# Kernel tuning notes

Measured on AMD Instinct MI355X. Metric: run time of the kernel, lower is better.

Reference implementation:

```python
import jax, jax.numpy as jnp
import numpy as np

EMB = 1024
HID = 1536
NE = 8


def setup_inputs() -> dict:
    key = jax.random.key(0)
    ks = jax.random.split(key, 8)
    B, N, E, H, ne = 4, 2048, EMB, HID, NE
    s = 1.0 / np.sqrt(E)
    sh = 1.0 / np.sqrt(H)
    return {
        "x": jax.random.normal(ks[0], (B, N, E), dtype=jnp.float32),
        "Wr": jax.random.uniform(ks[1], (E, ne), minval=-s, maxval=s, dtype=jnp.float32),
        "br": jax.random.uniform(ks[2], (ne,), minval=-s, maxval=s, dtype=jnp.float32),
        "W1": jax.random.uniform(ks[3], (ne, E, H), minval=-s, maxval=s, dtype=jnp.float32),
        "b1": jax.random.uniform(ks[4], (ne, H), minval=-s, maxval=s, dtype=jnp.float32),
        "W2": jax.random.uniform(ks[5], (ne, H, E), minval=-sh, maxval=sh, dtype=jnp.float32),
        "b2": jax.random.uniform(ks[6], (ne, E), minval=-sh, maxval=sh, dtype=jnp.float32),
        "k": 2,
    }


def reference(x, Wr, br, W1, b1, W2, b2, k):
    B, N, E = x.shape
    T = B * N
    ne = Wr.shape[1]
    flat = x.reshape(T, E)
    logits = flat @ Wr + br                      # [T, ne]
    _, topk_idx = jax.lax.top_k(logits, k)       # [T, k]
    # counts[t, e] = number of top-k slots of token t assigned to expert e
    counts = jax.nn.one_hot(topk_idx, ne, dtype=flat.dtype).sum(axis=1)  # [T, ne]
    out = jnp.zeros_like(flat)
    for e in range(ne):  # small fixed loop over experts (structurally distinct weights)
        h = jax.nn.gelu(flat @ W1[e] + b1[e], approximate=False)  # torch nn.GELU = exact erf
        y = h @ W2[e] + b2[e]
        out = out + counts[:, e:e + 1] * y
    out = out / k
    return out.reshape(B, N, E)
```

## Files before the change

### kernel.cpp

```cpp
#include <hip/hip_runtime.h>
#include <hip/hip_bf16.h>
#include <math.h>

#define T_TOK 8192
#define EMB   1024
#define HID   1536
#define NE    8

typedef float  floatx4 __attribute__((ext_vector_type(4)));
typedef __bf16 bf16x8  __attribute__((ext_vector_type(8)));

#define WS_COUNTS   0
#define WS_OFFSETS  1024
#define WS_TOKMAP   8192
#define WS_TOKLIST  270336
#define WS_YBUF     532480
#define WS_W1T      34086912
#define WS_W2T      59252736
#define WS_H        84418560
#define WS_NEEDED   135143424

__device__ __forceinline__ bool wave_sniff_f32(const void* p, int nelem) {
  const unsigned* w = (const unsigned*)p;
  int nw = nelem >> 1; if (nw > 256) nw = 256;
  const int lane = threadIdx.x & 63;
  int pl = 0, nz = 0;
  for (int i = lane; i < nw; i += 64) {
    unsigned v = w[i];
    if (v) { nz++; unsigned ex = (v >> 23) & 255; if (ex >= 100 && ex <= 150) pl++; }
  }
#pragma unroll
  for (int off = 32; off; off >>= 1) { pl += __shfl_xor(pl, off, 64); nz += __shfl_xor(nz, off, 64); }
  return 2 * pl > nz;
}

__device__ __forceinline__ float eload(const void* p, size_t idx, bool f32) {
  return f32 ? ((const float*)p)[idx] : (float)(((const __bf16*)p)[idx]);
}

__device__ __forceinline__ void glds16(const void* g, void* l) {
  __builtin_amdgcn_global_load_lds(
      (const __attribute__((address_space(1))) unsigned int*)g,
      (__attribute__((address_space(3))) unsigned int*)l, 16, 0, 0);
}

__device__ __forceinline__ void transpose_tile(const void* in, __bf16* out,
                                               int K, int N, bool f32,
                                               int t, int lane) {
  const int ntile = N / 64;
  const int e  = t / 384;
  const int r  = t % 384;
  const int kb = r / ntile;
  const int nb = r % ntile;
  const size_t eoff = (size_t)e * (size_t)K * (size_t)N;
  const int k0 = kb * 64 + (lane >> 3) * 8;
  const int n0 = nb * 64 + (lane & 7) * 8;

  if (f32) {
    floatx4 a0[8], a1[8];
#pragma unroll
    for (int i = 0; i < 8; ++i) {
      const float* g = (const float*)in + eoff + (size_t)(k0 + i) * N + n0;
      a0[i] = *(const floatx4*)g;
      a1[i] = *(const floatx4*)(g + 4);
    }
#pragma unroll
    for (int j = 0; j < 8; ++j) {
      bf16x8 o;
#pragma unroll
      for (int i = 0; i < 8; ++i)
        o[i] = (__bf16)(j < 4 ? a0[i][j] : a1[i][j - 4]);
      *(bf16x8*)(out + eoff + (size_t)(n0 + j) * K + k0) = o;
    }
  } else {
    bf16x8 a[8];
#pragma unroll
    for (int i = 0; i < 8; ++i)
      a[i] = *(const bf16x8*)((const __bf16*)in + eoff + (size_t)(k0 + i) * N + n0);
#pragma unroll
    for (int j = 0; j < 8; ++j) {
      bf16x8 o;
#pragma unroll
      for (int i = 0; i < 8; ++i) o[i] = a[i][j];
      *(bf16x8*)(out + eoff + (size_t)(n0 + j) * K + k0) = o;
    }
  }
}

__global__ __launch_bounds__(256)
void prep_kernel(const void* __restrict__ W1, __bf16* __restrict__ w1t,
                 const void* __restrict__ x, const void* __restrict__ Wr,
                 const void* __restrict__ br, const int* __restrict__ kptr,
                 int* __restrict__ tokmap, __bf16* __restrict__ xbf) {
  const int bid = blockIdx.x;
  const int tid = threadIdx.x;
  const int wave = tid >> 6;
  const int lane = tid & 63;

  if (bid < 768) {
    const bool f32 = wave_sniff_f32(W1, NE * EMB * HID);
    transpose_tile(W1, w1t, EMB, HID, f32, bid * 4 + wave, lane);
    return;
  }

  const bool xf32  = wave_sniff_f32(x, T_TOK * EMB);
  const bool wrf32 = wave_sniff_f32(Wr, EMB * NE);
  const bool brf32 = wave_sniff_f32(br, NE);
  const int t = (bid - 768) * 4 + wave;

  float xv[16];
  {
    size_t base = (size_t)t * EMB + lane * 16;
    if (xf32) {
      const float* g = (const float*)x + base;
#pragma unroll
      for (int c = 0; c < 4; ++c) {
        float4 v = *(const float4*)(g + c * 4);
        xv[c * 4 + 0] = v.x; xv[c * 4 + 1] = v.y; xv[c * 4 + 2] = v.z; xv[c * 4 + 3] = v.w;
      }
    } else {
      bf16x8 u = *(const bf16x8*)((const __bf16*)x + base);
      bf16x8 v = *(const bf16x8*)((const __bf16*)x + base + 8);
#pragma unroll
      for (int j = 0; j < 8; ++j) { xv[j] = (float)u[j]; xv[8 + j] = (float)v[j]; }
    }
  }
  {
    bf16x8 o0, o1;
#pragma unroll
    for (int j = 0; j < 8; ++j) { o0[j] = (__bf16)xv[j]; o1[j] = (__bf16)xv[8 + j]; }
    __bf16* xo = xbf + (size_t)t * EMB + lane * 16;
    *(bf16x8*)xo = o0;
    *(bf16x8*)(xo + 8) = o1;
  }
  float acc[NE];
#pragma unroll
  for (int e = 0; e < NE; ++e) acc[e] = 0.f;
  if (wrf32) {
#pragma unroll
    for (int j = 0; j < 16; ++j) {
      const float* wr = (const float*)Wr + (size_t)(lane * 16 + j) * NE;
#pragma unroll
      for (int e = 0; e < NE; ++e) acc[e] += xv[j] * wr[e];
    }
  } else {
#pragma unroll
    for (int j = 0; j < 16; ++j) {
      bf16x8 wr = *(const bf16x8*)((const __bf16*)Wr + (size_t)(lane * 16 + j) * NE);
#pragma unroll
      for (int e = 0; e < NE; ++e) acc[e] += xv[j] * (float)wr[e];
    }
  }
#pragma unroll
  for (int e = 0; e < NE; ++e) {
#pragma unroll
    for (int off = 32; off > 0; off >>= 1)
      acc[e] += __shfl_xor(acc[e], off, 64);
  }
  if (lane == 0) {
    int k = kptr[0];
    if (k < 1) k = 1; if (k > NE) k = NE;
    float lg[NE];
#pragma unroll
    for (int e = 0; e < NE; ++e) lg[e] = acc[e] + eload(br, e, brf32);
    for (int s = 0; s < k; ++s) {
      int bi = 0; float bv = lg[0];
#pragma unroll
      for (int e = 1; e < NE; ++e) { if (lg[e] > bv) { bv = lg[e]; bi = e; } }
      lg[bi] = -3.0e38f;
      tokmap[t * 8 + s] = bi;
    }
  }
}

__global__ __launch_bounds__(1024)
void bin_kernel(const int* __restrict__ kptr, int* __restrict__ tokmap,
                int* __restrict__ tok_list, int* __restrict__ counts,
                int* __restrict__ offsets) {
  __shared__ int lcnt[NE];
  __shared__ int soff[NE + 1];
  const int tid = threadIdx.x;
  if (tid < NE) lcnt[tid] = 0;
  __syncthreads();
  int k = kptr[0];
  if (k < 1) k = 1; if (k > NE) k = NE;
  for (int t = tid; t < T_TOK; t += 1024) {
    for (int s = 0; s < k; ++s) {
      int e = tokmap[t * 8 + s] & 7;
      int pos = atomicAdd(&lcnt[e], 1);
      tok_list[e * T_TOK + pos] = t;
      tokmap[t * 8 + s] = (e << 16) | pos;
    }
  }
  __syncthreads();
  if (tid == 0) {
    int s = 0;
    for (int e = 0; e < NE; ++e) { soff[e] = s; s += lcnt[e]; }
    soff[NE] = s;
  }
  __syncthreads();
  if (tid < NE) counts[tid] = lcnt[tid];
  if (tid <= NE) offsets[tid] = soff[tid];
  for (int e = 0; e < NE; ++e) {
    const int c = lcnt[e];
    const int end = (c + 127) & ~127;
    for (int i = c + tid; i < end; i += 1024) tok_list[e * T_TOK + i] = 0;
  }
}

__global__ __launch_bounds__(256, 4)
void gemm1_kernel(const __bf16* __restrict__ xbf, const __bf16* __restrict__ w1t,
                  const void* __restrict__ b1, const int* __restrict__ counts,
                  const int* __restrict__ offsets, const int* __restrict__ tok_list,
                  __bf16* __restrict__ hbuf,
                  const void* __restrict__ W2, __bf16* __restrict__ w2t) {
  const int bid = blockIdx.x;
  const int lane = threadIdx.x & 63;

  if (bid < 768) {
    const bool f32 = wave_sniff_f32(W2, NE * EMB * HID);
    transpose_tile(W2, w2t, HID, EMB, f32, bid * 4 + (threadIdx.x >> 6), lane);
    return;
  }

  const int flat = bid - 768;
  const int e   = flat & 7;
  const int idx = flat >> 3;
  const int g   = idx / 12;
  const int nT  = idx % 12;
  const int cnt = counts[e];
  const bool b1f32 = wave_sniff_f32(b1, NE * HID);

  __shared__ __align__(16) __bf16 As[128 * 64];
  __shared__ __align__(16) __bf16 Bs[128 * 64];

  const int wave = threadIdx.x >> 6;
  const int lrow = lane >> 3;
  const int cgs  = (lane & 7) ^ lrow;

  int Rst[4];
#pragma unroll
  for (int q = 0; q < 4; ++q) Rst[q] = (q * 4 + wave) * 8 + lrow;

  const __bf16* pB[4];
#pragma unroll
  for (int q = 0; q < 4; ++q)
    pB[q] = w1t + ((size_t)e * HID + nT * 128 + Rst[q]) * EMB + cgs * 8;

  const int wm = (wave & 1) * 64;
  const int wn = (wave >> 1) * 64;
  const int fr = lane & 15;
  const int fc = lane >> 4;
  int aOff0[4], aOff1[4], bOff0[4], bOff1[4];
#pragma unroll
  for (int i = 0; i < 4; ++i) {
    int R = wm + i * 16 + fr;
    aOff0[i] = R * 128 + (((fc)     ^ (R & 7)) << 4);
    aOff1[i] = R * 128 + (((fc + 4) ^ (R & 7)) << 4);
  }
#pragma unroll
  for (int j = 0; j < 4; ++j) {
    int R = wn + j * 16 + fr;
    bOff0[j] = R * 128 + (((fc)     ^ (R & 7)) << 4);
    bOff1[j] = R * 128 + (((fc + 4) ^ (R & 7)) << 4);
  }

  const int colBase = nT * 128 + wn + fr;
  float bv[4];
#pragma unroll
  for (int j = 0; j < 4; ++j) bv[j] = eload(b1, (size_t)e * HID + colBase + j * 16, b1f32);

  for (int mT = g; mT * 128 < cnt; mT += 16) {
    const __bf16* pA[4];
#pragma unroll
    for (int q = 0; q < 4; ++q) {
      const int tok = tok_list[e * T_TOK + mT * 128 + Rst[q]];
      pA[q] = xbf + (size_t)tok * EMB + cgs * 8;
    }

    floatx4 acc[4][4];
#pragma unroll
    for (int i = 0; i < 4; ++i)
#pragma unroll
      for (int j = 0; j < 4; ++j) acc[i][j] = (floatx4){0.f, 0.f, 0.f, 0.f};

    for (int kb = 0; kb < EMB / 64; ++kb) {
      __syncthreads();
#pragma unroll
      for (int q = 0; q < 4; ++q) glds16(pA[q] + (size_t)kb * 64, As + (q * 4 + wave) * 512);
#pragma unroll
      for (int q = 0; q < 4; ++q) glds16(pB[q] + (size_t)kb * 64, Bs + (q * 4 + wave) * 512);
      __syncthreads();
      bf16x8 af[4], bfr[4];
#pragma unroll
      for (int i = 0; i < 4; ++i) af[i]  = *(const bf16x8*)((const char*)As + aOff0[i]);
#pragma unroll
      for (int j = 0; j < 4; ++j) bfr[j] = *(const bf16x8*)((const char*)Bs + bOff0[j]);
#pragma unroll
      for (int i = 0; i < 4; ++i)
#pragma unroll
        for (int j = 0; j < 4; ++j)
          acc[i][j] = __builtin_amdgcn_mfma_f32_16x16x32_bf16(af[i], bfr[j], acc[i][j], 0, 0, 0);
#pragma unroll
      for (int i = 0; i < 4; ++i) af[i]  = *(const bf16x8*)((const char*)As + aOff1[i]);
#pragma unroll
      for (int j = 0; j < 4; ++j) bfr[j] = *(const bf16x8*)((const char*)Bs + bOff1[j]);
#pragma unroll
      for (int i = 0; i < 4; ++i)
#pragma unroll
        for (int j = 0; j < 4; ++j)
          acc[i][j] = __builtin_amdgcn_mfma_f32_16x16x32_bf16(af[i], bfr[j], acc[i][j], 0, 0, 0);
    }

    const int hBase = offsets[e] + mT * 128;
#pragma unroll
    for (int i = 0; i < 4; ++i) {
      const int rowLoc = wm + i * 16 + fc * 4;
#pragma unroll
      for (int r = 0; r < 4; ++r) {
        const int row = rowLoc + r;
        if (mT * 128 + row < cnt) {
          __bf16* hp = hbuf + (size_t)(hBase + row) * HID + colBase;
#pragma unroll
          for (int j = 0; j < 4; ++j) {
            float v = acc[i][j][r] + bv[j];
            float gl = 0.5f * v * (1.0f + erff(v * 0.70710678118654752f));
            hp[j * 16] = (__bf16)gl;
          }
        }
      }
    }
  }
}

__global__ __launch_bounds__(256, 4)
void gemm2_kernel(const __bf16* __restrict__ hbuf, const __bf16* __restrict__ w2t,
                  const void* __restrict__ b2, const int* __restrict__ counts,
                  const int* __restrict__ offsets, __bf16* __restrict__ ybuf) {
  const int flat = blockIdx.x;
  const int e   = flat & 7;
  const int idx = flat >> 3;
  const int g   = idx >> 3;
  const int nT  = idx & 7;
  const int cnt = counts[e];
  const bool b2f32 = wave_sniff_f32(b2, NE * EMB);

  __shared__ __align__(16) __bf16 As[128 * 64];
  __shared__ __align__(16) __bf16 Bs[128 * 64];

  const int wave = threadIdx.x >> 6;
  const int lane = threadIdx.x & 63;
  const int lrow = lane >> 3;
  const int cgs  = (lane & 7) ^ lrow;

  int Rst[4];
#pragma unroll
  for (int q = 0; q < 4; ++q) Rst[q] = (q * 4 + wave) * 8 + lrow;

  const __bf16* pB[4];
#pragma unroll
  for (int q = 0; q < 4; ++q)
    pB[q] = w2t + ((size_t)e * EMB + nT * 128 + Rst[q]) * HID + cgs * 8;

  const int wm = (wave & 1) * 64;
  const int wn = (wave >> 1) * 64;
  const int fr = lane & 15;
  const int fc = lane >> 4;
  int aOff0[4], aOff1[4], bOff0[4], bOff1[4];
#pragma unroll
  for (int i = 0; i < 4; ++i) {
    int R = wm + i * 16 + fr;
    aOff0[i] = R * 128 + (((fc)     ^ (R & 7)) << 4);
    aOff1[i] = R * 128 + (((fc + 4) ^ (R & 7)) << 4);
  }
#pragma unroll
  for (int j = 0; j < 4; ++j) {
    int R = wn + j * 16 + fr;
    bOff0[j] = R * 128 + (((fc)     ^ (R & 7)) << 4);
    bOff1[j] = R * 128 + (((fc + 4) ^ (R & 7)) << 4);
  }

  const int colBase = nT * 128 + wn + fr;
  float bv[4];
#pragma unroll
  for (int j = 0; j < 4; ++j) bv[j] = eload(b2, (size_t)e * EMB + colBase + j * 16, b2f32);

  for (int mT = g; mT * 128 < cnt; mT += 16) {
    const int rowBase = offsets[e] + mT * 128;
    const __bf16* pA[4];
#pragma unroll
    for (int q = 0; q < 4; ++q)
      pA[q] = hbuf + (size_t)(rowBase + Rst[q]) * HID + cgs * 8;

    floatx4 acc[4][4];
#pragma unroll
    for (int i = 0; i < 4; ++i)
#pragma unroll
      for (int j = 0; j < 4; ++j) acc[i][j] = (floatx4){0.f, 0.f, 0.f, 0.f};

    for (int kb = 0; kb < HID / 64; ++kb) {
      __syncthreads();
#pragma unroll
      for (int q = 0; q < 4; ++q) glds16(pA[q] + (size_t)kb * 64, As + (q * 4 + wave) * 512);
#pragma unroll
      for (int q = 0; q < 4; ++q) glds16(pB[q] + (size_t)kb * 64, Bs + (q * 4 + wave) * 512);
      __syncthreads();
      bf16x8 af[4], bfr[4];
#pragma unroll
      for (int i = 0; i < 4; ++i) af[i]  = *(const bf16x8*)((const char*)As + aOff0[i]);
#pragma unroll
      for (int j = 0; j < 4; ++j) bfr[j] = *(const bf16x8*)((const char*)Bs + bOff0[j]);
#pragma unroll
      for (int i = 0; i < 4; ++i)
#pragma unroll
        for (int j = 0; j < 4; ++j)
          acc[i][j] = __builtin_amdgcn_mfma_f32_16x16x32_bf16(af[i], bfr[j], acc[i][j], 0, 0, 0);
#pragma unroll
      for (int i = 0; i < 4; ++i) af[i]  = *(const bf16x8*)((const char*)As + aOff1[i]);
#pragma unroll
      for (int j = 0; j < 4; ++j) bfr[j] = *(const bf16x8*)((const char*)Bs + bOff1[j]);
#pragma unroll
      for (int i = 0; i < 4; ++i)
#pragma unroll
        for (int j = 0; j < 4; ++j)
          acc[i][j] = __builtin_amdgcn_mfma_f32_16x16x32_bf16(af[i], bfr[j], acc[i][j], 0, 0, 0);
    }

#pragma unroll
    for (int i = 0; i < 4; ++i) {
      const int rowLoc = wm + i * 16 + fc * 4;
#pragma unroll
      for (int r = 0; r < 4; ++r) {
        const int row = rowLoc + r;
        if (mT * 128 + row < cnt) {
          __bf16* yp = ybuf + (size_t)(rowBase + row) * EMB + colBase;
#pragma unroll
          for (int j = 0; j < 4; ++j)
            yp[j * 16] = (__bf16)(acc[i][j][r] + bv[j]);
        }
      }
    }
  }
}

__global__ __launch_bounds__(256)
void combine_kernel(const __bf16* __restrict__ ybuf, const int* __restrict__ tokmap,
                    const int* __restrict__ offsets, const int* __restrict__ kptr,
                    const void* __restrict__ x, void* __restrict__ out) {
  const bool f32 = wave_sniff_f32(x, T_TOK * EMB);
  const int wave = threadIdx.x >> 6;
  const int lane = threadIdx.x & 63;
  const int t = blockIdx.x * 4 + wave;
  int k = kptr[0];
  if (k < 1) k = 1; if (k > NE) k = NE;
  const float invk = 1.0f / (float)k;
  int rows[NE];
  for (int s = 0; s < k; ++s) {
    int m = tokmap[t * 8 + s];
    rows[s] = offsets[(m >> 16) & 7] + (m & 0xFFFF);
  }
#pragma unroll
  for (int c = 0; c < 2; ++c) {
    const int i = c * 512 + lane * 8;
    float a[8];
#pragma unroll
    for (int j = 0; j < 8; ++j) a[j] = 0.f;
    for (int s = 0; s < k; ++s) {
      bf16x8 y = *(const bf16x8*)(ybuf + (size_t)rows[s] * EMB + i);
#pragma unroll
      for (int j = 0; j < 8; ++j) a[j] += (float)y[j];
    }
    if (f32) {
      float* op = (float*)out + (size_t)t * EMB + i;
      float4 u = {a[0] * invk, a[1] * invk, a[2] * invk, a[3] * invk};
      float4 v = {a[4] * invk, a[5] * invk, a[6] * invk, a[7] * invk};
      *(float4*)op = u;
      *(float4*)(op + 4) = v;
    } else {
      bf16x8 o;
#pragma unroll
      for (int j = 0; j < 8; ++j) o[j] = (__bf16)(a[j] * invk);
      *(bf16x8*)((__bf16*)out + (size_t)t * EMB + i) = o;
    }
  }
}

extern "C" void kernel_launch(void* const* d_in, const int* in_sizes, int n_in,
                              void* d_out, int out_size, void* d_ws, size_t ws_size,
                              hipStream_t stream) {
  (void)in_sizes; (void)n_in; (void)out_size;
  if (ws_size < (size_t)WS_NEEDED) return;

  const void* x  = d_in[0];
  const void* Wr = d_in[1];
  const void* br = d_in[2];
  const void* W1 = d_in[3];
  const void* b1 = d_in[4];
  const void* W2 = d_in[5];
  const void* b2 = d_in[6];
  const int* kptr = (const int*)d_in[7];

  char* ws = (char*)d_ws;
  int*    counts   = (int*)(ws + WS_COUNTS);
  int*    offsets  = (int*)(ws + WS_OFFSETS);
  int*    tokmap   = (int*)(ws + WS_TOKMAP);
  int*    tok_list = (int*)(ws + WS_TOKLIST);
  __bf16* ybuf     = (__bf16*)(ws + WS_YBUF);
  __bf16* xbf      = (__bf16*)(ws + WS_YBUF);
  __bf16* w1t      = (__bf16*)(ws + WS_W1T);
  __bf16* w2t      = (__bf16*)(ws + WS_W2T);
  __bf16* hbuf     = (__bf16*)(ws + WS_H);

  prep_kernel<<<dim3(768 + T_TOK / 4), 256, 0, stream>>>(
      W1, w1t, x, Wr, br, kptr, tokmap, xbf);

  bin_kernel<<<dim3(1), 1024, 0, stream>>>(kptr, tokmap, tok_list, counts, offsets);

  gemm1_kernel<<<dim3(768 + 8 * 16 * 12), 256, 0, stream>>>(
      xbf, w1t, b1, counts, offsets, tok_list, hbuf, W2, w2t);

  gemm2_kernel<<<dim3(8 * 16 * 8), 256, 0, stream>>>(
      hbuf, w2t, b2, counts, offsets, ybuf);

  combine_kernel<<<dim3(T_TOK / 4), 256, 0, stream>>>(ybuf, tokmap, offsets, kptr, x, d_out);
}
```

Baseline: 372.4 us.

## Double-buffer LDS tiles with async prefetch two stages ahead in both GEMMs

Both expert GEMM kernels now keep two LDS buffers. The direct global-to-LDS loads for k-block kb+2 are issued while block kb is computed, gated by vmcnt waits instead of full syncthreads. All fragment reads now happen up front, followed by an lgkmcnt wait, and the MFMA section runs at raised wave priority. The aim is to hide global load latency behind MFMA work, at the cost of doubling LDS use and lowering the occupancy hint from 4 to 2 blocks per SM.

```diff
diff --git a/kernel.cpp b/kernel.cpp
--- a/kernel.cpp
+++ b/kernel.cpp
@@ -208,7 +208,12 @@
   }
 }
 
-__global__ __launch_bounds__(256, 4)
+
+#define GATE(N_) asm volatile("s_waitcnt vmcnt(" #N_ ")" ::: "memory")
+#define LGKM0()  do { asm volatile("s_waitcnt lgkmcnt(0)" ::: "memory"); \
+                      __builtin_amdgcn_sched_barrier(0); } while (0)
+
+__global__ __launch_bounds__(256, 2)
 void gemm1_kernel(const __bf16* __restrict__ xbf, const __bf16* __restrict__ w1t,
                   const void* __restrict__ b1, const int* __restrict__ counts,
                   const int* __restrict__ offsets, const int* __restrict__ tok_list,
@@ -231,8 +236,7 @@
   const int cnt = counts[e];
   const bool b1f32 = wave_sniff_f32(b1, NE * HID);
 
-  __shared__ __align__(16) __bf16 As[128 * 64];
-  __shared__ __align__(16) __bf16 Bs[128 * 64];
+  __shared__ __align__(16) __bf16 L[2][2 * 128 * 64];
 
   const int wave = threadIdx.x >> 6;
   const int lrow = lane >> 3;
@@ -261,8 +265,8 @@
 #pragma unroll
   for (int j = 0; j < 4; ++j) {
     int R = wn + j * 16 + fr;
-    bOff0[j] = R * 128 + (((fc)     ^ (R & 7)) << 4);
-    bOff1[j] = R * 128 + (((fc + 4) ^ (R & 7)) << 4);
+    bOff0[j] = 16384 + R * 128 + (((fc)     ^ (R & 7)) << 4);
+    bOff1[j] = 16384 + R * 128 + (((fc + 4) ^ (R & 7)) << 4);
   }
 
   const int colBase = nT * 128 + wn + fr;
@@ -278,39 +282,55 @@
       pA[q] = xbf + (size_t)tok * EMB + cgs * 8;
     }
 
+#define STAGE1(BUF, KO) do {                                             \
+    __bf16* _d = &L[BUF][0] + (size_t)(4 * 0);                           \
+    _Pragma("unroll")                                                    \
+    for (int _q = 0; _q < 4; ++_q) glds16(pA[_q] + (KO), &L[BUF][(_q * 4 + wave) * 512]); \
+    _Pragma("unroll")                                                    \
+    for (int _q = 0; _q < 4; ++_q) glds16(pB[_q] + (KO), &L[BUF][8192 + (_q * 4 + wave) * 512]); \
+    (void)_d;                                                            \
+  } while (0)
+
     floatx4 acc[4][4];
 #pragma unroll
     for (int i = 0; i < 4; ++i)
 #pragma unroll
       for (int j = 0; j < 4; ++j) acc[i][j] = (floatx4){0.f, 0.f, 0.f, 0.f};
 
-    for (int kb = 0; kb < EMB / 64; ++kb) {
-      __syncthreads();
-#pragma unroll
-      for (int q = 0; q < 4; ++q) glds16(pA[q] + (size_t)kb * 64, As + (q * 4 + wave) * 512);
-#pragma unroll
-      for (int q = 0; q < 4; ++q) glds16(pB[q] + (size_t)kb * 64, Bs + (q * 4 + wave) * 512);
-      __syncthreads();
-      bf16x8 af[4], bfr[4];
-#pragma unroll
-      for (int i = 0; i < 4; ++i) af[i]  = *(const bf16x8*)((const char*)As + aOff0[i]);
-#pragma unroll
-      for (int j = 0; j < 4; ++j) bfr[j] = *(const bf16x8*)((const char*)Bs + bOff0[j]);
+    STAGE1(0, 0);
+    STAGE1(1, 64);
+    const int nk = EMB / 64;
+    for (int kb = 0; kb < nk; ++kb) {
+      if (kb < nk - 1) GATE(8); else GATE(0);
+      __builtin_amdgcn_s_barrier();
+      const int cur = kb & 1;
+      const char* s = (const char*)&L[cur][0];
+      bf16x8 a0[4], a1[4], b0[4], b1v[4];
+#pragma unroll
+      for (int i = 0; i < 4; ++i) a0[i]  = *(const bf16x8*)(s + aOff0[i]);
+#pragma unroll
+      for (int i = 0; i < 4; ++i) a1[i]  = *(const bf16x8*)(s + aOff1[i]);
+#pragma unroll
+      for (int j = 0; j < 4; ++j) b0[j]  = *(const bf16x8*)(s + bOff0[j]);
+#pragma unroll
+      for (int j = 0; j < 4; ++j) b1v[j] = *(const bf16x8*)(s + bOff1[j]);
+      LGKM0();
+      __builtin_amdgcn_s_barrier();
+      if (kb + 2 < nk) STAGE1(cur, (size_t)(kb + 2) * 64);
+      __builtin_amdgcn_s_setprio(1);
 #pragma unroll
       for (int i = 0; i < 4; ++i)
 #pragma unroll
         for (int j = 0; j < 4; ++j)
-          acc[i][j] = __builtin_amdgcn_mfma_f32_16x16x32_bf16(af[i], bfr[j], acc[i][j], 0, 0, 0);
-#pragma unroll
-      for (int i = 0; i < 4; ++i) af[i]  = *(const bf16x8*)((const char*)As + aOff1[i]);
-#pragma unroll
-      for (int j = 0; j < 4; ++j) bfr[j] = *(const bf16x8*)((const char*)Bs + bOff1[j]);
+          acc[i][j] = __builtin_amdgcn_mfma_f32_16x16x32_bf16(a0[i], b0[j], acc[i][j], 0, 0, 0);
 #pragma unroll
       for (int i = 0; i < 4; ++i)
 #pragma unroll
         for (int j = 0; j < 4; ++j)
-          acc[i][j] = __builtin_amdgcn_mfma_f32_16x16x32_bf16(af[i], bfr[j], acc[i][j], 0, 0, 0);
-    }
+          acc[i][j] = __builtin_amdgcn_mfma_f32_16x16x32_bf16(a1[i], b1v[j], acc[i][j], 0, 0, 0);
+      __builtin_amdgcn_s_setprio(0);
+    }
+#undef STAGE1
 
     const int hBase = offsets[e] + mT * 128;
 #pragma unroll
@@ -333,7 +353,7 @@
   }
 }
 
-__global__ __launch_bounds__(256, 4)
+__global__ __launch_bounds__(256, 2)
 void gemm2_kernel(const __bf16* __restrict__ hbuf, const __bf16* __restrict__ w2t,
                   const void* __restrict__ b2, const int* __restrict__ counts,
                   const int* __restrict__ offsets, __bf16* __restrict__ ybuf) {
@@ -345,8 +365,7 @@
   const int cnt = counts[e];
   const bool b2f32 = wave_sniff_f32(b2, NE * EMB);
 
-  __shared__ __align__(16) __bf16 As[128 * 64];
-  __shared__ __align__(16) __bf16 Bs[128 * 64];
+  __shared__ __align__(16) __bf16 L[2][2 * 128 * 64];
 
   const int wave = threadIdx.x >> 6;
   const int lane = threadIdx.x & 63;
@@ -376,8 +395,8 @@
 #pragma unroll
   for (int j = 0; j < 4; ++j) {
     int R = wn + j * 16 + fr;
-    bOff0[j] = R * 128 + (((fc)     ^ (R & 7)) << 4);
-    bOff1[j] = R * 128 + (((fc + 4) ^ (R & 7)) << 4);
+    bOff0[j] = 16384 + R * 128 + (((fc)     ^ (R & 7)) << 4);
+    bOff1[j] = 16384 + R * 128 + (((fc + 4) ^ (R & 7)) << 4);
   }
 
   const int colBase = nT * 128 + wn + fr;
@@ -392,39 +411,53 @@
     for (int q = 0; q < 4; ++q)
       pA[q] = hbuf + (size_t)(rowBase + Rst[q]) * HID + cgs * 8;
 
+#define STAGE2(BUF, KO) do {                                             \
+    _Pragma("unroll")                                                    \
+    for (int _q = 0; _q < 4; ++_q) glds16(pA[_q] + (KO), &L[BUF][(_q * 4 + wave) * 512]); \
+    _Pragma("unroll")                                                    \
+    for (int _q = 0; _q < 4; ++_q) glds16(pB[_q] + (KO), &L[BUF][8192 + (_q * 4 + wave) * 512]); \
+  } while (0)
+
     floatx4 acc[4][4];
 #pragma unroll
     for (int i = 0; i < 4; ++i)
 #pragma unroll
       for (int j = 0; j < 4; ++j) acc[i][j] = (floatx4){0.f, 0.f, 0.f, 0.f};
 
-    for (int kb = 0; kb < HID / 64; ++kb) {
-      __syncthreads();
-#pragma unroll
-      for (int q = 0; q < 4; ++q) glds16(pA[q] + (size_t)kb * 64, As + (q * 4 + wave) * 512);
-#pragma unroll
-      for (int q = 0; q < 4; ++q) glds16(pB[q] + (size_t)kb * 64, Bs + (q * 4 + wave) * 512);
-      __syncthreads();
-      bf16x8 af[4], bfr[4];
-#pragma unroll
-      for (int i = 0; i < 4; ++i) af[i]  = *(const bf16x8*)((const char*)As + aOff0[i]);
-#pragma unroll
-      for (int j = 0; j < 4; ++j) bfr[j] = *(const bf16x8*)((const char*)Bs + bOff0[j]);
+    STAGE2(0, 0);
+    STAGE2(1, 64);
+    const int nk = HID / 64;
+    for (int kb = 0; kb < nk; ++kb) {
+      if (kb < nk - 1) GATE(8); else GATE(0);
+      __builtin_amdgcn_s_barrier();
+      const int cur = kb & 1;
+      const char* s = (const char*)&L[cur][0];
+      bf16x8 a0[4], a1[4], b0[4], b1v[4];
+#pragma unroll
+      for (int i = 0; i < 4; ++i) a0[i]  = *(const bf16x8*)(s + aOff0[i]);
+#pragma unroll
+      for (int i = 0; i < 4; ++i) a1[i]  = *(const bf16x8*)(s + aOff1[i]);
+#pragma unroll
+      for (int j = 0; j < 4; ++j) b0[j]  = *(const bf16x8*)(s + bOff0[j]);
+#pragma unroll
+      for (int j = 0; j < 4; ++j) b1v[j] = *(const bf16x8*)(s + bOff1[j]);
+      LGKM0();
+      __builtin_amdgcn_s_barrier();
+      if (kb + 2 < nk) STAGE2(cur, (size_t)(kb + 2) * 64);
+      __builtin_amdgcn_s_setprio(1);
 #pragma unroll
       for (int i = 0; i < 4; ++i)
 #pragma unroll
         for (int j = 0; j < 4; ++j)
-          acc[i][j] = __builtin_amdgcn_mfma_f32_16x16x32_bf16(af[i], bfr[j], acc[i][j], 0, 0, 0);
-#pragma unroll
-      for (int i = 0; i < 4; ++i) af[i]  = *(const bf16x8*)((const char*)As + aOff1[i]);
-#pragma unroll
-      for (int j = 0; j < 4; ++j) bfr[j] = *(const bf16x8*)((const char*)Bs + bOff1[j]);
+          acc[i][j] = __builtin_amdgcn_mfma_f32_16x16x32_bf16(a0[i], b0[j], acc[i][j], 0, 0, 0);
 #pragma unroll
       for (int i = 0; i < 4; ++i)
 #pragma unroll
         for (int j = 0; j < 4; ++j)
-          acc[i][j] = __builtin_amdgcn_mfma_f32_16x16x32_bf16(af[i], bfr[j], acc[i][j], 0, 0, 0);
-    }
+          acc[i][j] = __builtin_amdgcn_mfma_f32_16x16x32_bf16(a1[i], b1v[j], acc[i][j], 0, 0, 0);
+      __builtin_amdgcn_s_setprio(0);
+    }
+#undef STAGE2
 
 #pragma unroll
     for (int i = 0; i < 4; ++i) {
```

Result: no change. 377.5 us (+1.4%).
